# Performance work log

Hardware: AMD Instinct MI355X
Metric: run time of the kernel (lower is better)

## Reference

```python
import jax, jax.numpy as jnp
import numpy as np
from jax import lax

D = 96          # voxel grid side
N = 131072      # active voxels
C = 128         # channels
EPS = 1e-4
SLOPE_INNER = 0.05      # nn.LeakyReLU(0.05)
SLOPE_OUT = 1.0 / 3.0   # scn.LeakyReLU() default leakiness


def _build_nbr():
    rng = np.random.default_rng(0)
    lin = rng.choice(D ** 3, size=N, replace=False)
    coords = np.stack(np.unravel_index(lin, (D, D, D)), axis=1)  # [N,3]
    lut = -np.ones(D ** 3, dtype=np.int64)
    lut[lin] = np.arange(N)
    nbr = np.full((N, 27), -1, dtype=np.int64)
    k = 0
    for dx in (-1, 0, 1):
        for dy in (-1, 0, 1):
            for dz in (-1, 0, 1):
                nc = coords + np.array([dx, dy, dz])
                valid = ((nc >= 0) & (nc < D)).all(axis=1)
                li = nc[valid, 0] * D * D + nc[valid, 1] * D + nc[valid, 2]
                nbr[valid, k] = lut[li]
                k += 1
    return nbr


def setup_inputs() -> dict:
    key = jax.random.key(0)
    ks = jax.random.split(key, 4)
    ws = 1.0 / np.sqrt(27 * C)
    return {
        "features": jax.random.normal(ks[0], (N, C), jnp.float32),
        "nbr_idx": jnp.asarray(_build_nbr()),
        "w1": jax.random.normal(ks[1], (27, C, C), jnp.float32) * ws,
        "w2": jax.random.normal(ks[2], (27, C, C), jnp.float32) * ws,
        "w3": jax.random.normal(ks[3], (27, C, C), jnp.float32) * ws,
        "g1": jnp.ones((C,), jnp.float32), "b1": jnp.zeros((C,), jnp.float32),
        "g2": jnp.ones((C,), jnp.float32), "b2": jnp.zeros((C,), jnp.float32),
        "g3": jnp.ones((C,), jnp.float32), "b3": jnp.zeros((C,), jnp.float32),
    }


def _subm_conv(feat, nbr, W):
    # feat [N,Cin], nbr [N,27] (-1 = no active neighbor), W [27,Cin,Cout]
    mask = nbr >= 0
    safe = jnp.where(mask, nbr, 0)
    acc0 = jnp.zeros((feat.shape[0], W.shape[-1]), feat.dtype)

    def step(acc, inp):
        idx, m, Wk = inp  # idx [N], m [N], Wk [Cin,Cout]
        g = feat[idx] * m[:, None].astype(feat.dtype)  # gather + mask
        return acc + g @ Wk, None

    out, _ = lax.scan(step, acc0, (safe.T, mask.T, W))
    return out


def _bn(x, g, b):
    # BatchNorm1d with batch stats (track_running_stats=False), biased var
    mu = x.mean(axis=0)
    var = x.var(axis=0)
    return (x - mu) * lax.rsqrt(var + EPS) * g + b


def _lrelu(x, slope):
    return jnp.where(x >= 0, x, slope * x)


def reference(features, nbr_idx, w1, w2, w3, g1, b1, g2, b2, g3, b3):
    x = _lrelu(_bn(_subm_conv(features, nbr_idx, w1), g1, b1), SLOPE_INNER)
    res = x
    x = _lrelu(_bn(_subm_conv(x, nbr_idx, w2), g2, b2), SLOPE_INNER)
    x = _bn(_subm_conv(x, nbr_idx, w3), g3, b3)
    return _lrelu(x + res, SLOPE_OUT)
```

## Files before the change

kernel.cpp:

```cpp
#include <hip/hip_runtime.h>
#include <hip/hip_bf16.h>
#include <stdint.h>

#define NVOX 131072
#define CCH  128
#define EPSV 1e-4f

typedef __bf16 bf16_t;
typedef bf16_t bf16x8 __attribute__((ext_vector_type(8)));
typedef bf16_t bf16x4 __attribute__((ext_vector_type(4)));
typedef float  f32x4  __attribute__((ext_vector_type(4)));

__device__ __forceinline__ void async16(void* lds, const void* g) {
    __builtin_amdgcn_global_load_lds(
        (const __attribute__((address_space(1))) uint32_t*)g,
        (__attribute__((address_space(3))) uint32_t*)lds, 16, 0, 0);
}

__global__ void k_prep_feat(const float* __restrict__ f, bf16_t* __restrict__ fb) {
    int i = blockIdx.x * 256 + threadIdx.x;
    const float4* f4 = (const float4*)f;
    float4 v = f4[i];
    bf16x4 o;
    o[0] = (bf16_t)v.x; o[1] = (bf16_t)v.y; o[2] = (bf16_t)v.z; o[3] = (bf16_t)v.w;
    ((bf16x4*)fb)[i] = o;
}

__global__ void k_prep_misc(bf16_t* featb, bf16_t* xb1, bf16_t* xb2, float* stats) {
    int t = threadIdx.x;
    if (t < 128) {
        featb[(size_t)NVOX * CCH + t] = (bf16_t)0.0f;
        xb1[(size_t)NVOX * CCH + t]   = (bf16_t)0.0f;
        xb2[(size_t)NVOX * CCH + t]   = (bf16_t)0.0f;
    }
    for (int i = t; i < 768; i += 256) stats[i] = 0.0f;
}

__global__ void k_prep_w(const float* __restrict__ w0, const float* __restrict__ w1,
                         const float* __restrict__ w2, bf16_t* __restrict__ wbt) {
    int blk = blockIdx.x;
    int layer = blk / 27, k = blk % 27;
    const float* w = (layer == 0 ? w0 : (layer == 1 ? w1 : w2)) + k * 16384;
    __shared__ bf16_t tile[128][132];
    for (int e = threadIdx.x; e < 16384; e += 256) {
        int ci = e >> 7, co = e & 127;
        tile[co][ci] = (bf16_t)w[e];
    }
    __syncthreads();
    bf16_t* out = wbt + (size_t)blk * 16384;
    for (int e = threadIdx.x; e < 16384; e += 256) {
        int co = e >> 7, ci = e & 127;
        out[e] = tile[co][ci];
    }
}

__global__ __launch_bounds__(256, 3) void k_conv(
        const bf16_t* __restrict__ featb,
        const bf16_t* __restrict__ wbt,
        const int* __restrict__ nbr,
        float* __restrict__ out,
        float* __restrict__ stat)
{
    __shared__ uint32_t offs[27 * 128];
    __shared__ bf16_t smA[128 * 32];
    __shared__ bf16_t smB[128 * 32];
    __shared__ float ssum[128], ssq[128];

    const int tid = threadIdx.x;
    const int m0 = blockIdx.x << 7;

    if (tid < 128) { ssum[tid] = 0.0f; ssq[tid] = 0.0f; }

    for (int e = tid; e < 27 * 128; e += 256) {
        int row = e / 27, k = e - row * 27;
        int idx = nbr[(size_t)(m0 + row) * 27 + k];
        offs[(k << 7) + row] = ((uint32_t)(idx < 0 ? NVOX : idx)) << 8;
    }
    __syncthreads();

    const int l = tid & 63, w = tid >> 6;
    const int wm = w >> 1, wn = w & 1;
    const int lrow = l & 15, lq = l >> 4;

    const int srow = (w << 4) + (l >> 2);
    const int ssub = (l & 3) << 4;

    char* dstA0 = (char*)smA + (w << 10);
    char* dstA1 = (char*)smA + 4096 + (w << 10);
    char* dstB0 = (char*)smB + (w << 10);
    char* dstB1 = (char*)smB + 4096 + (w << 10);

    const char* fbase = (const char*)featb;
    const char* wbase = (const char*)wbt;

    f32x4 acc[4][4] = {};

    for (int k = 0; k < 27; ++k) {
        uint32_t offA0 = offs[(k << 7) + srow];
        uint32_t offA1 = offs[(k << 7) + srow + 64];
        const char* wk = wbase + ((size_t)k << 15);
        #pragma unroll
        for (int c = 0; c < 4; ++c) {
            const int cb = c << 6;
            __syncthreads();
            async16(dstA0, fbase + offA0 + cb + ssub);
            async16(dstA1, fbase + offA1 + cb + ssub);
            async16(dstB0, wk + (srow << 8) + cb + ssub);
            async16(dstB1, wk + ((srow + 64) << 8) + cb + ssub);
            __syncthreads();

            bf16x8 af[4], bfr[4];
            #pragma unroll
            for (int i = 0; i < 4; ++i) {
                af[i]  = *(const bf16x8*)((const char*)smA +
                          ((((wm << 6) + (i << 4) + lrow)) << 6) + (lq << 4));
                bfr[i] = *(const bf16x8*)((const char*)smB +
                          ((((wn << 6) + (i << 4) + lrow)) << 6) + (lq << 4));
            }
            #pragma unroll
            for (int i = 0; i < 4; ++i)
                #pragma unroll
                for (int j = 0; j < 4; ++j)
                    acc[i][j] = __builtin_amdgcn_mfma_f32_16x16x32_bf16(
                        af[i], bfr[j], acc[i][j], 0, 0, 0);
        }
    }

    float csum[4] = {0, 0, 0, 0}, csq[4] = {0, 0, 0, 0};
    #pragma unroll
    for (int j = 0; j < 4; ++j) {
        int col = (wn << 6) + (j << 4) + lrow;
        #pragma unroll
        for (int i = 0; i < 4; ++i) {
            int grow = m0 + (wm << 6) + (i << 4) + (lq << 2);
            #pragma unroll
            for (int r = 0; r < 4; ++r) {
                float v = acc[i][j][r];
                out[(size_t)(grow + r) * CCH + col] = v;
                csum[j] += v;
                csq[j]  += v * v;
            }
        }
    }
    #pragma unroll
    for (int j = 0; j < 4; ++j) {
        csum[j] += __shfl_xor(csum[j], 16, 64);
        csum[j] += __shfl_xor(csum[j], 32, 64);
        csq[j]  += __shfl_xor(csq[j], 16, 64);
        csq[j]  += __shfl_xor(csq[j], 32, 64);
    }
    if (lq == 0) {
        #pragma unroll
        for (int j = 0; j < 4; ++j) {
            int col = (wn << 6) + (j << 4) + lrow;
            atomicAdd(&ssum[col], csum[j]);
            atomicAdd(&ssq[col],  csq[j]);
        }
    }
    __syncthreads();
    if (tid < 128) {
        atomicAdd(&stat[tid],       ssum[tid]);
        atomicAdd(&stat[128 + tid], ssq[tid]);
    }
}

__global__ void k_bnact(const float* __restrict__ x, const float* __restrict__ stat,
                        const float* __restrict__ g, const float* __restrict__ b,
                        bf16_t* __restrict__ out, float slope) {
    __shared__ float sc[128], sh[128];
    int tid = threadIdx.x;
    if (tid < 128) {
        float mu  = stat[tid] * (1.0f / NVOX);
        float var = stat[128 + tid] * (1.0f / NVOX) - mu * mu;
        float inv = rsqrtf(var + EPSV);
        float s = g[tid] * inv;
        sc[tid] = s;
        sh[tid] = b[tid] - mu * s;
    }
    __syncthreads();
    int i = blockIdx.x * 256 + tid;
    float4 v = ((const float4*)x)[i];
    int c = (i << 2) & 127;
    float y0 = v.x * sc[c]     + sh[c];
    float y1 = v.y * sc[c + 1] + sh[c + 1];
    float y2 = v.z * sc[c + 2] + sh[c + 2];
    float y3 = v.w * sc[c + 3] + sh[c + 3];
    y0 = y0 >= 0.0f ? y0 : slope * y0;
    y1 = y1 >= 0.0f ? y1 : slope * y1;
    y2 = y2 >= 0.0f ? y2 : slope * y2;
    y3 = y3 >= 0.0f ? y3 : slope * y3;
    bf16x4 o;
    o[0] = (bf16_t)y0; o[1] = (bf16_t)y1; o[2] = (bf16_t)y2; o[3] = (bf16_t)y3;
    ((bf16x4*)out)[i] = o;
}

__global__ void k_final(const float* __restrict__ x, const float* __restrict__ stat,
                        const float* __restrict__ g, const float* __restrict__ b,
                        const bf16_t* __restrict__ res, float* __restrict__ out) {
    __shared__ float sc[128], sh[128];
    int tid = threadIdx.x;
    if (tid < 128) {
        float mu  = stat[tid] * (1.0f / NVOX);
        float var = stat[128 + tid] * (1.0f / NVOX) - mu * mu;
        float inv = rsqrtf(var + EPSV);
        float s = g[tid] * inv;
        sc[tid] = s;
        sh[tid] = b[tid] - mu * s;
    }
    __syncthreads();
    int i = blockIdx.x * 256 + tid;
    float4 v = ((const float4*)x)[i];
    bf16x4 r = ((const bf16x4*)res)[i];
    int c = (i << 2) & 127;
    float y0 = v.x * sc[c]     + sh[c]     + (float)r[0];
    float y1 = v.y * sc[c + 1] + sh[c + 1] + (float)r[1];
    float y2 = v.z * sc[c + 2] + sh[c + 2] + (float)r[2];
    float y3 = v.w * sc[c + 3] + sh[c + 3] + (float)r[3];
    const float k3 = 1.0f / 3.0f;
    y0 = y0 >= 0.0f ? y0 : k3 * y0;
    y1 = y1 >= 0.0f ? y1 : k3 * y1;
    y2 = y2 >= 0.0f ? y2 : k3 * y2;
    y3 = y3 >= 0.0f ? y3 : k3 * y3;
    float4 o; o.x = y0; o.y = y1; o.z = y2; o.w = y3;
    ((float4*)out)[i] = o;
}

extern "C" void kernel_launch(void* const* d_in, const int* in_sizes, int n_in,
                              void* d_out, int out_size, void* d_ws, size_t ws_size,
                              hipStream_t stream) {
    (void)in_sizes; (void)n_in; (void)out_size; (void)ws_size;
    const float* features = (const float*)d_in[0];
    const int*   nbr      = (const int*)d_in[1];
    const float* w1 = (const float*)d_in[2];
    const float* w2 = (const float*)d_in[3];
    const float* w3 = (const float*)d_in[4];
    const float* g1 = (const float*)d_in[5];
    const float* b1 = (const float*)d_in[6];
    const float* g2 = (const float*)d_in[7];
    const float* b2 = (const float*)d_in[8];
    const float* g3 = (const float*)d_in[9];
    const float* b3 = (const float*)d_in[10];

    char* ws = (char*)d_ws;
    const size_t SZ_FB = (size_t)(NVOX + 1) * CCH * 2;
    bf16_t* featb    = (bf16_t*)(ws);
    bf16_t* xb1      = (bf16_t*)(ws + SZ_FB);
    bf16_t* xb2      = (bf16_t*)(ws + 2 * SZ_FB);
    float*  conv_out = (float*)(ws + 3 * SZ_FB);
    bf16_t* wbt      = (bf16_t*)(ws + 3 * SZ_FB + (size_t)NVOX * CCH * 4);
    float*  stats    = (float*)(ws + 3 * SZ_FB + (size_t)NVOX * CCH * 4
                                + (size_t)3 * 27 * 128 * 128 * 2);

    k_prep_feat<<<16384, 256, 0, stream>>>(features, featb);
    k_prep_misc<<<1, 256, 0, stream>>>(featb, xb1, xb2, stats);
    k_prep_w<<<81, 256, 0, stream>>>(w1, w2, w3, wbt);

    k_conv<<<1024, 256, 0, stream>>>(featb, wbt, nbr, conv_out, stats);
    k_bnact<<<16384, 256, 0, stream>>>(conv_out, stats, g1, b1, xb1, 0.05f);

    k_conv<<<1024, 256, 0, stream>>>(xb1, wbt + (size_t)27 * 16384, nbr, conv_out, stats + 256);
    k_bnact<<<16384, 256, 0, stream>>>(conv_out, stats + 256, g2, b2, xb2, 0.05f);

    k_conv<<<1024, 256, 0, stream>>>(xb2, wbt + (size_t)2 * 27 * 16384, nbr, conv_out, stats + 512);
    k_final<<<16384, 256, 0, stream>>>(conv_out, stats + 512, g3, b3, xb1, (float*)d_out);
}
```

Measured before the change: 548.9 us.

## Compact neighbor rules per block and skip empty offsets in sparse conv

Adds a preprocessing kernel that builds, per 128-voxel block and kernel offset, a compacted list of valid neighbor rows. The conv kernel then gathers only those rows, runs MFMA on 16-row tiles and scatter-accumulates into an fp32 LDS accumulator, so work on missing neighbors is skipped. Conv outputs are stored as bf16 instead of fp32, halving intermediate traffic for the BN kernels, which now process 8 elements per thread. The cost is lower occupancy (512 threads, large LDS use per block), LDS scatter-add overhead, and extra rounding of pre-BN activations.

```diff
diff --git a/kernel.cpp b/kernel.cpp
--- a/kernel.cpp
+++ b/kernel.cpp
@@ -26,12 +26,12 @@
     ((bf16x4*)fb)[i] = o;
 }
 
-__global__ void k_prep_misc(bf16_t* featb, bf16_t* xb1, bf16_t* xb2, float* stats) {
+__global__ void k_prep_misc(bf16_t* featb, bf16_t* y1, bf16_t* y2, float* stats) {
     int t = threadIdx.x;
     if (t < 128) {
         featb[(size_t)NVOX * CCH + t] = (bf16_t)0.0f;
-        xb1[(size_t)NVOX * CCH + t]   = (bf16_t)0.0f;
-        xb2[(size_t)NVOX * CCH + t]   = (bf16_t)0.0f;
+        y1[(size_t)NVOX * CCH + t]    = (bf16_t)0.0f;
+        y2[(size_t)NVOX * CCH + t]    = (bf16_t)0.0f;
     }
     for (int i = t; i < 768; i += 256) stats[i] = 0.0f;
 }
@@ -54,107 +54,156 @@
     }
 }
 
-__global__ __launch_bounds__(256, 3) void k_conv(
-        const bf16_t* __restrict__ featb,
+__global__ void k_prep_rule(const int* __restrict__ nbr, unsigned* __restrict__ rule,
+                            int* __restrict__ cntTab) {
+    __shared__ int snbr[128 * 27];
+    __shared__ int c0s[4];
+    const int b = blockIdx.x, tid = threadIdx.x, m0 = b << 7;
+    for (int i = tid; i < 128 * 27; i += 256) snbr[i] = nbr[(size_t)m0 * 27 + i];
+    __syncthreads();
+    const int w = tid >> 6, l = tid & 63;
+    for (int k = 0; k < 27; ++k) {
+        int idx = 0; bool valid = false;
+        if (tid < 128) { idx = snbr[tid * 27 + k]; valid = idx >= 0; }
+        unsigned long long m = __ballot(valid);
+        if (l == 0) c0s[w] = (int)__popcll(m);
+        __syncthreads();
+        int base = (w == 1) ? c0s[0] : 0;
+        int total = c0s[0] + c0s[1];
+        int prefix = (int)__popcll(m & ((1ull << l) - 1ull));
+        unsigned* rk = rule + ((size_t)b * 27 + k) * 128;
+        if (valid) rk[base + prefix] = ((unsigned)tid << 18) | (unsigned)idx;
+        int nr = ((total + 15) >> 4) << 4;
+        if (tid < nr - total) rk[total + tid] = (unsigned)NVOX;
+        if (tid == 0) cntTab[b * 27 + k] = total;
+        __syncthreads();
+    }
+}
+
+__global__ __launch_bounds__(512, 1) void k_conv_sp(
+        const bf16_t* __restrict__ xin,
         const bf16_t* __restrict__ wbt,
-        const int* __restrict__ nbr,
-        float* __restrict__ out,
+        const unsigned* __restrict__ rule,
+        const int* __restrict__ cntTab,
+        bf16_t* __restrict__ yout,
         float* __restrict__ stat)
 {
-    __shared__ uint32_t offs[27 * 128];
-    __shared__ bf16_t smA[128 * 32];
-    __shared__ bf16_t smB[128 * 32];
+    __shared__ __align__(16) float  accf[128 * 128];
+    __shared__ __align__(16) bf16_t smB[128 * 128];
+    __shared__ __align__(16) bf16_t smA[128 * 128];
+    __shared__ unsigned short rowLds[128];
     __shared__ float ssum[128], ssq[128];
 
     const int tid = threadIdx.x;
-    const int m0 = blockIdx.x << 7;
-
-    if (tid < 128) { ssum[tid] = 0.0f; ssq[tid] = 0.0f; }
-
-    for (int e = tid; e < 27 * 128; e += 256) {
-        int row = e / 27, k = e - row * 27;
-        int idx = nbr[(size_t)(m0 + row) * 27 + k];
-        offs[(k << 7) + row] = ((uint32_t)(idx < 0 ? NVOX : idx)) << 8;
-    }
-    __syncthreads();
-
-    const int l = tid & 63, w = tid >> 6;
-    const int wm = w >> 1, wn = w & 1;
+    const int b = blockIdx.x;
+    const int w = tid >> 6, l = tid & 63;
     const int lrow = l & 15, lq = l >> 4;
 
-    const int srow = (w << 4) + (l >> 2);
-    const int ssub = (l & 3) << 4;
-
-    char* dstA0 = (char*)smA + (w << 10);
-    char* dstA1 = (char*)smA + 4096 + (w << 10);
-    char* dstB0 = (char*)smB + (w << 10);
-    char* dstB1 = (char*)smB + 4096 + (w << 10);
-
-    const char* fbase = (const char*)featb;
-    const char* wbase = (const char*)wbt;
-
-    f32x4 acc[4][4] = {};
+    for (int i = tid; i < 128 * 128 / 4; i += 512)
+        ((f32x4*)accf)[i] = (f32x4){0.f, 0.f, 0.f, 0.f};
+    if (tid < 128) { ssum[tid] = 0.f; ssq[tid] = 0.f; }
+
+    const char* xb = (const char*)xin;
+    const unsigned* ruleB = rule + (size_t)b * 27 * 128;
 
     for (int k = 0; k < 27; ++k) {
-        uint32_t offA0 = offs[(k << 7) + srow];
-        uint32_t offA1 = offs[(k << 7) + srow + 64];
-        const char* wk = wbase + ((size_t)k << 15);
+        const int cnt = cntTab[b * 27 + k];
+        if (cnt == 0) continue;
+        const int ntiles = (cnt + 15) >> 4;
+        const int nchunks = ntiles << 8;
+
+        __syncthreads();
+
+        const char* wk = (const char*)wbt + ((size_t)k << 15);
+        #pragma unroll
+        for (int r = 0; r < 4; ++r) {
+            int c = (r << 9) + tid;
+            int row = c >> 4, s = c & 15;
+            int sg = s ^ (row & 15);
+            async16((char*)smB + ((size_t)c << 4), wk + (row << 8) + (sg << 4));
+        }
+        const unsigned* rk = ruleB + (k << 7);
+        for (int c0 = 0; c0 < nchunks; c0 += 512) {
+            if ((c0 + (w << 6)) < nchunks) {
+                int c = c0 + tid;
+                int row = c >> 4, s = c & 15;
+                unsigned e = rk[row];
+                unsigned gidx = e & 0x3FFFFu;
+                int sg = s ^ (row & 15);
+                async16((char*)smA + ((size_t)c << 4),
+                        xb + ((size_t)gidx << 8) + (sg << 4));
+                if (s == 0) rowLds[row] = (unsigned short)(e >> 18);
+            }
+        }
+        __syncthreads();
+
+        bf16x8 bfr[4];
         #pragma unroll
         for (int c = 0; c < 4; ++c) {
-            const int cb = c << 6;
-            __syncthreads();
-            async16(dstA0, fbase + offA0 + cb + ssub);
-            async16(dstA1, fbase + offA1 + cb + ssub);
-            async16(dstB0, wk + (srow << 8) + cb + ssub);
-            async16(dstB1, wk + ((srow + 64) << 8) + cb + ssub);
-            __syncthreads();
-
-            bf16x8 af[4], bfr[4];
-            #pragma unroll
-            for (int i = 0; i < 4; ++i) {
-                af[i]  = *(const bf16x8*)((const char*)smA +
-                          ((((wm << 6) + (i << 4) + lrow)) << 6) + (lq << 4));
-                bfr[i] = *(const bf16x8*)((const char*)smB +
-                          ((((wn << 6) + (i << 4) + lrow)) << 6) + (lq << 4));
+            int slot = ((c << 2) + lq) ^ lrow;
+            bfr[c] = *(const bf16x8*)((const char*)smB +
+                      (((w << 4) + lrow) << 8) + (slot << 4));
+        }
+        f32x4 tacc[8];
+        #pragma unroll
+        for (int t = 0; t < 8; ++t) {
+            if (t < ntiles) {
+                f32x4 a = {0.f, 0.f, 0.f, 0.f};
+                #pragma unroll
+                for (int c = 0; c < 4; ++c) {
+                    int slot = ((c << 2) + lq) ^ lrow;
+                    bf16x8 af = *(const bf16x8*)((const char*)smA +
+                                 (((t << 4) + lrow) << 8) + (slot << 4));
+                    a = __builtin_amdgcn_mfma_f32_16x16x32_bf16(af, bfr[c], a, 0, 0, 0);
+                }
+                tacc[t] = a;
             }
-            #pragma unroll
-            for (int i = 0; i < 4; ++i)
+        }
+        const int col = (w << 4) + lrow;
+        #pragma unroll
+        for (int t = 0; t < 8; ++t) {
+            if (t < ntiles) {
                 #pragma unroll
-                for (int j = 0; j < 4; ++j)
-                    acc[i][j] = __builtin_amdgcn_mfma_f32_16x16x32_bf16(
-                        af[i], bfr[j], acc[i][j], 0, 0, 0);
-        }
-    }
-
-    float csum[4] = {0, 0, 0, 0}, csq[4] = {0, 0, 0, 0};
+                for (int r = 0; r < 4; ++r) {
+                    int ridx = (t << 4) + (lq << 2) + r;
+                    if (ridx < cnt) {
+                        int row = rowLds[ridx];
+                        accf[(row << 7) + col] += tacc[t][r];
+                    }
+                }
+            }
+        }
+    }
+    __syncthreads();
+
+    float ps[8] = {0,0,0,0,0,0,0,0}, pq[8] = {0,0,0,0,0,0,0,0};
+    const int cb = (tid & 15) << 3;
+    bf16_t* yrow = yout + ((size_t)b << 7) * CCH;
     #pragma unroll
-    for (int j = 0; j < 4; ++j) {
-        int col = (wn << 6) + (j << 4) + lrow;
-        #pragma unroll
-        for (int i = 0; i < 4; ++i) {
-            int grow = m0 + (wm << 6) + (i << 4) + (lq << 2);
-            #pragma unroll
-            for (int r = 0; r < 4; ++r) {
-                float v = acc[i][j][r];
-                out[(size_t)(grow + r) * CCH + col] = v;
-                csum[j] += v;
-                csq[j]  += v * v;
-            }
-        }
+    for (int r = 0; r < 4; ++r) {
+        int row = (r << 5) + (tid >> 4);
+        const float* ap = accf + (row << 7) + cb;
+        bf16x8 o;
+        #pragma unroll
+        for (int i = 0; i < 8; ++i) {
+            float v = ap[i];
+            o[i] = (bf16_t)v;
+            ps[i] += v; pq[i] += v * v;
+        }
+        ((bf16x8*)yrow)[(row << 4) + (tid & 15)] = o;
     }
     #pragma unroll
-    for (int j = 0; j < 4; ++j) {
-        csum[j] += __shfl_xor(csum[j], 16, 64);
-        csum[j] += __shfl_xor(csum[j], 32, 64);
-        csq[j]  += __shfl_xor(csq[j], 16, 64);
-        csq[j]  += __shfl_xor(csq[j], 32, 64);
+    for (int i = 0; i < 8; ++i) {
+        ps[i] += __shfl_xor(ps[i], 16, 64);
+        ps[i] += __shfl_xor(ps[i], 32, 64);
+        pq[i] += __shfl_xor(pq[i], 16, 64);
+        pq[i] += __shfl_xor(pq[i], 32, 64);
     }
     if (lq == 0) {
         #pragma unroll
-        for (int j = 0; j < 4; ++j) {
-            int col = (wn << 6) + (j << 4) + lrow;
-            atomicAdd(&ssum[col], csum[j]);
-            atomicAdd(&ssq[col],  csq[j]);
+        for (int i = 0; i < 8; ++i) {
+            atomicAdd(&ssum[cb + i], ps[i]);
+            atomicAdd(&ssq[cb + i],  pq[i]);
         }
     }
     __syncthreads();
@@ -164,7 +213,7 @@
     }
 }
 
-__global__ void k_bnact(const float* __restrict__ x, const float* __restrict__ stat,
+__global__ void k_bnact(const bf16_t* __restrict__ x, const float* __restrict__ stat,
                         const float* __restrict__ g, const float* __restrict__ b,
                         bf16_t* __restrict__ out, float slope) {
     __shared__ float sc[128], sh[128];
@@ -179,22 +228,19 @@
     }
     __syncthreads();
     int i = blockIdx.x * 256 + tid;
-    float4 v = ((const float4*)x)[i];
-    int c = (i << 2) & 127;
-    float y0 = v.x * sc[c]     + sh[c];
-    float y1 = v.y * sc[c + 1] + sh[c + 1];
-    float y2 = v.z * sc[c + 2] + sh[c + 2];
-    float y3 = v.w * sc[c + 3] + sh[c + 3];
-    y0 = y0 >= 0.0f ? y0 : slope * y0;
-    y1 = y1 >= 0.0f ? y1 : slope * y1;
-    y2 = y2 >= 0.0f ? y2 : slope * y2;
-    y3 = y3 >= 0.0f ? y3 : slope * y3;
-    bf16x4 o;
-    o[0] = (bf16_t)y0; o[1] = (bf16_t)y1; o[2] = (bf16_t)y2; o[3] = (bf16_t)y3;
-    ((bf16x4*)out)[i] = o;
-}
-
-__global__ void k_final(const float* __restrict__ x, const float* __restrict__ stat,
+    bf16x8 v = ((const bf16x8*)x)[i];
+    int c = (i << 3) & 127;
+    bf16x8 o;
+    #pragma unroll
+    for (int j = 0; j < 8; ++j) {
+        float y = (float)v[j] * sc[c + j] + sh[c + j];
+        y = y >= 0.0f ? y : slope * y;
+        o[j] = (bf16_t)y;
+    }
+    ((bf16x8*)out)[i] = o;
+}
+
+__global__ void k_final(const bf16_t* __restrict__ x, const float* __restrict__ stat,
                         const float* __restrict__ g, const float* __restrict__ b,
                         const bf16_t* __restrict__ res, float* __restrict__ out) {
     __shared__ float sc[128], sh[128];
@@ -209,20 +255,21 @@
     }
     __syncthreads();
     int i = blockIdx.x * 256 + tid;
-    float4 v = ((const float4*)x)[i];
-    bf16x4 r = ((const bf16x4*)res)[i];
-    int c = (i << 2) & 127;
-    float y0 = v.x * sc[c]     + sh[c]     + (float)r[0];
-    float y1 = v.y * sc[c + 1] + sh[c + 1] + (float)r[1];
-    float y2 = v.z * sc[c + 2] + sh[c + 2] + (float)r[2];
-    float y3 = v.w * sc[c + 3] + sh[c + 3] + (float)r[3];
+    bf16x8 v = ((const bf16x8*)x)[i];
+    bf16x8 r8 = ((const bf16x8*)res)[i];
+    int c = (i << 3) & 127;
     const float k3 = 1.0f / 3.0f;
-    y0 = y0 >= 0.0f ? y0 : k3 * y0;
-    y1 = y1 >= 0.0f ? y1 : k3 * y1;
-    y2 = y2 >= 0.0f ? y2 : k3 * y2;
-    y3 = y3 >= 0.0f ? y3 : k3 * y3;
-    float4 o; o.x = y0; o.y = y1; o.z = y2; o.w = y3;
-    ((float4*)out)[i] = o;
+    float4 o0, o1;
+    float* op = (float*)&o0;
+    #pragma unroll
+    for (int j = 0; j < 8; ++j) {
+        float y = (float)v[j] * sc[c + j] + sh[c + j] + (float)r8[j];
+        y = y >= 0.0f ? y : k3 * y;
+        if (j < 4) ((float*)&o0)[j] = y; else ((float*)&o1)[j - 4] = y;
+    }
+    (void)op;
+    ((float4*)out)[2 * i]     = o0;
+    ((float4*)out)[2 * i + 1] = o1;
 }
 
 extern "C" void kernel_launch(void* const* d_in, const int* in_sizes, int n_in,
@@ -243,24 +290,26 @@
 
     char* ws = (char*)d_ws;
     const size_t SZ_FB = (size_t)(NVOX + 1) * CCH * 2;
-    bf16_t* featb    = (bf16_t*)(ws);
-    bf16_t* xb1      = (bf16_t*)(ws + SZ_FB);
-    bf16_t* xb2      = (bf16_t*)(ws + 2 * SZ_FB);
-    float*  conv_out = (float*)(ws + 3 * SZ_FB);
-    bf16_t* wbt      = (bf16_t*)(ws + 3 * SZ_FB + (size_t)NVOX * CCH * 4);
-    float*  stats    = (float*)(ws + 3 * SZ_FB + (size_t)NVOX * CCH * 4
-                                + (size_t)3 * 27 * 128 * 128 * 2);
+    bf16_t*   featb  = (bf16_t*)(ws);
+    bf16_t*   y1     = (bf16_t*)(ws + SZ_FB);
+    bf16_t*   y2     = (bf16_t*)(ws + 2 * SZ_FB);
+    bf16_t*   y3     = (bf16_t*)(ws + 3 * SZ_FB);
+    bf16_t*   wbt    = (bf16_t*)(ws + 4 * SZ_FB);
+    unsigned* rule   = (unsigned*)(ws + 4 * SZ_FB + 2654208);
+    int*      cntTab = (int*)(ws + 4 * SZ_FB + 2654208 + 14155776);
+    float*    stats  = (float*)(ws + 4 * SZ_FB + 2654208 + 14155776 + 110592);
 
     k_prep_feat<<<16384, 256, 0, stream>>>(features, featb);
-    k_prep_misc<<<1, 256, 0, stream>>>(featb, xb1, xb2, stats);
+    k_prep_misc<<<1, 256, 0, stream>>>(featb, y1, y2, stats);
     k_prep_w<<<81, 256, 0, stream>>>(w1, w2, w3, wbt);
-
-    k_conv<<<1024, 256, 0, stream>>>(featb, wbt, nbr, conv_out, stats);
-    k_bnact<<<16384, 256, 0, stream>>>(conv_out, stats, g1, b1, xb1, 0.05f);
-
-    k_conv<<<1024, 256, 0, stream>>>(xb1, wbt + (size_t)27 * 16384, nbr, conv_out, stats + 256);
-    k_bnact<<<16384, 256, 0, stream>>>(conv_out, stats + 256, g2, b2, xb2, 0.05f);
-
-    k_conv<<<1024, 256, 0, stream>>>(xb2, wbt + (size_t)2 * 27 * 16384, nbr, conv_out, stats + 512);
-    k_final<<<16384, 256, 0, stream>>>(conv_out, stats + 512, g3, b3, xb1, (float*)d_out);
-}
+    k_prep_rule<<<1024, 256, 0, stream>>>(nbr, rule, cntTab);
+
+    k_conv_sp<<<1024, 512, 0, stream>>>(featb, wbt, rule, cntTab, y1, stats);
+    k_bnact<<<8192, 256, 0, stream>>>(y1, stats, g1, b1, y1, 0.05f);
+
+    k_conv_sp<<<1024, 512, 0, stream>>>(y1, wbt + (size_t)27 * 16384, rule, cntTab, y2, stats + 256);
+    k_bnact<<<8192, 256, 0, stream>>>(y2, stats + 256, g2, b2, y2, 0.05f);
+
+    k_conv_sp<<<1024, 512, 0, stream>>>(y2, wbt + (size_t)54 * 16384, rule, cntTab, y3, stats + 512);
+    k_final<<<8192, 256, 0, stream>>>(y3, stats + 512, g3, b3, y1, (float*)d_out);
+}
```

Measured after the change: 913.2 us. +66.4%, slower.
